# Optimization experiments

Hardware: AMD Instinct MI355X
Metric: run time of the kernel (lower is better)

The kernel has to match this reference:

```python
import jax, jax.numpy as jnp
import numpy as np

B, S = 4096, 256
D = 32  # output_size // 4


def setup_inputs() -> dict:
    key = jax.random.key(0)
    ks = jax.random.split(key, 32)
    # continuous features
    cont_p = jax.random.normal(ks[0], (B, S, 3), dtype=jnp.float32)
    cont_c = jax.random.normal(ks[1], (B, S, 2), dtype=jnp.float32)
    # categorical features, per-column vocab sizes from Embedding tables
    vocabs_p = [2, 2, 2, 11, 34]
    cat_p = jnp.stack([
        jax.random.randint(ks[2 + i], (B, S), 0, v, dtype=jnp.int32)
        for i, v in enumerate(vocabs_p)], axis=2)
    vocabs_c = [19, 31]
    cat_c = jnp.stack([
        jax.random.randint(ks[7 + i], (B, S), 0, v, dtype=jnp.int32)
        for i, v in enumerate(vocabs_c)], axis=2)
    lengths = jax.random.randint(ks[9], (B,), 1, S + 1, dtype=jnp.int32)

    def lin(k, fan_in, fan_out):
        bound = 1.0 / np.sqrt(fan_in)
        kw, kb = jax.random.split(k)
        w = jax.random.uniform(kw, (fan_in, fan_out), jnp.float32, -bound, bound)
        b = jax.random.uniform(kb, (fan_out,), jnp.float32, -bound, bound)
        return w, b

    w_p1, b_p1 = lin(ks[10], 3, D)
    w_p2, b_p2 = lin(ks[11], D, D)
    w_c1, b_c1 = lin(ks[12], 2, D)
    w_c2, b_c2 = lin(ks[13], D, D)
    emb_gender = jax.random.normal(ks[14], (2, D), dtype=jnp.float32)
    emb_korean = jax.random.normal(ks[15], (2, D), dtype=jnp.float32)
    emb_primary = jax.random.normal(ks[16], (2, D), dtype=jnp.float32)
    emb_job = jax.random.normal(ks[17], (11, D), dtype=jnp.float32)
    emb_rep = jax.random.normal(ks[18], (34, D), dtype=jnp.float32)
    emb_place = jax.random.normal(ks[19], (19, D), dtype=jnp.float32)
    emb_add = jax.random.normal(ks[20], (31, D), dtype=jnp.float32)
    w_fc1, b_fc1 = lin(ks[21], 128, 64)
    w_fc2, b_fc2 = lin(ks[22], 64, 2)

    return dict(cont_p=cont_p, cont_c=cont_c, cat_p=cat_p, cat_c=cat_c,
                lengths=lengths,
                w_p1=w_p1, b_p1=b_p1, w_p2=w_p2, b_p2=b_p2,
                w_c1=w_c1, b_c1=b_c1, w_c2=w_c2, b_c2=b_c2,
                emb_gender=emb_gender, emb_korean=emb_korean,
                emb_primary=emb_primary, emb_job=emb_job, emb_rep=emb_rep,
                emb_place=emb_place, emb_add=emb_add,
                w_fc1=w_fc1, b_fc1=b_fc1, w_fc2=w_fc2, b_fc2=b_fc2)


def reference(cont_p, cont_c, cat_p, cat_c, lengths,
              w_p1, b_p1, w_p2, b_p2, w_c1, b_c1, w_c2, b_c2,
              emb_gender, emb_korean, emb_primary, emb_job, emb_rep,
              emb_place, emb_add, w_fc1, b_fc1, w_fc2, b_fc2):
    # small per-token MLPs on continuous features -> [B,S,D]
    hp = jax.nn.relu(cont_p @ w_p1 + b_p1) @ w_p2 + b_p2
    hc = jax.nn.relu(cont_c @ w_c1 + b_c1) @ w_c2 + b_c2
    # multi-table embedding lookups, averaged per group -> [B,S,D]
    ep = (emb_gender[cat_p[:, :, 0]] + emb_korean[cat_p[:, :, 1]] +
          emb_primary[cat_p[:, :, 2]] + emb_job[cat_p[:, :, 3]] +
          emb_rep[cat_p[:, :, 4]]) / 5.0
    ec = (emb_place[cat_c[:, :, 0]] + emb_add[cat_c[:, :, 1]]) / 2.0
    # concat order matches torch: (cat_p, cat_c, cont_p, cont_c) -> [B,S,128]
    x = jnp.concatenate([ep, ec, hp, hc], axis=2)
    # ragged mean pool over first lengths[i] positions (masked segment mean)
    mask = (jnp.arange(x.shape[1])[None, :] < lengths[:, None])
    pooled = jnp.sum(x * mask[:, :, None], axis=1) / lengths[:, None].astype(x.dtype)
    # head: relu(fc1) -> relu(fc2); dropout p=0.0 is identity
    h = jax.nn.relu(pooled @ w_fc1 + b_fc1)
    return jax.nn.relu(h @ w_fc2 + b_fc2)
```

## Files before the change

### kernel.cpp

```cpp
#include <hip/hip_runtime.h>


#define BDIM 64

__global__ __launch_bounds__(BDIM, 4)
void mlpreg_kernel(const float* __restrict__ cont_p,
                   const float* __restrict__ cont_c,
                   const int* __restrict__ cat_p,
                   const int* __restrict__ cat_c,
                   const int* __restrict__ lengths,
                   const float* __restrict__ w_p1, const float* __restrict__ b_p1,
                   const float* __restrict__ w_p2, const float* __restrict__ b_p2,
                   const float* __restrict__ w_c1, const float* __restrict__ b_c1,
                   const float* __restrict__ w_c2, const float* __restrict__ b_c2,
                   const float* __restrict__ emb_g,  const float* __restrict__ emb_k,
                   const float* __restrict__ emb_pr, const float* __restrict__ emb_j,
                   const float* __restrict__ emb_r,  const float* __restrict__ emb_pl,
                   const float* __restrict__ emb_a,
                   const float* __restrict__ w_fc1, const float* __restrict__ b_fc1,
                   const float* __restrict__ w_fc2, const float* __restrict__ b_fc2,
                   float* __restrict__ out)
{
    constexpr int S = 256;
    __shared__ int   hist[96];
    __shared__ float sAcc[64];
    __shared__ float sPool[128];

    const int lane = threadIdx.x;
    const int b = blockIdx.x;
    const int ch = lane & 31, h = lane >> 5;

    int L = lengths[b]; L = (L < 1) ? 1 : (L > S ? S : L);
    const float Lf = (float)L, invL = 1.0f / Lf;

    hist[lane] = 0;
    if (lane < 32) hist[64 + lane] = 0;

    const float wp0 = w_p1[ch], wp1 = w_p1[32 + ch], wp2 = w_p1[64 + ch], bp = b_p1[ch];
    const float wc0 = w_c1[ch], wc1 = w_c1[32 + ch], bc = b_c1[ch];

    int sg = 0, sk = 0, sp = 0;
    {
        const int*  kp = cat_p + (size_t)b * (S * 5);
        const int2* kc = (const int2*)(cat_c + (size_t)b * (S * 2));
        #pragma unroll 2
        for (int t = lane; t < L; t += 64) {
            int v0 = kp[5 * t], v1 = kp[5 * t + 1], v2 = kp[5 * t + 2],
                v3 = kp[5 * t + 3], v4 = kp[5 * t + 4];
            int2 q = kc[t];
            sg += v0; sk += v1; sp += v2;
            atomicAdd(&hist[v3], 1);
            atomicAdd(&hist[11 + v4], 1);
            atomicAdd(&hist[45 + q.x], 1);
            atomicAdd(&hist[64 + q.y], 1);
        }
    }

    float aP = 0.f, aC = 0.f;
    {
        const float* tp = cont_p + (size_t)b * (S * 3);
        const float* tc = cont_c + (size_t)b * (S * 2);
        #pragma unroll 4
        for (int t = h; t < L; t += 2) {
            float c0 = tp[3 * t], c1 = tp[3 * t + 1], c2 = tp[3 * t + 2];
            float2 d2 = *(const float2*)&tc[2 * t];
            aP += fmaxf(fmaf(c0, wp0, fmaf(c1, wp1, fmaf(c2, wp2, bp))), 0.f);
            aC += fmaxf(fmaf(d2.x, wc0, fmaf(d2.y, wc1, bc)), 0.f);
        }
    }
    aP += __shfl_xor(aP, 32);
    aC += __shfl_xor(aC, 32);
    #pragma unroll
    for (int d = 32; d; d >>= 1) {
        sg += __shfl_xor(sg, d); sk += __shfl_xor(sk, d); sp += __shfl_xor(sp, d);
    }

    sAcc[lane] = (h ? aC : aP) * invL;
    __syncthreads();

    float A;
    {
        float fg = (float)sg, fk = (float)sk, fp = (float)sp;
        float g0 = emb_g[ch],  g1 = emb_g[32 + ch];
        float k0 = emb_k[ch],  k1 = emb_k[32 + ch];
        float p0 = emb_pr[ch], p1 = emb_pr[32 + ch];
        A = fmaf(Lf - fg, g0, fg * g1) + fmaf(Lf - fk, k0, fk * k1)
          + fmaf(Lf - fp, p0, fp * p1);
        A = h ? 0.f : A;
    }
    {
        const float* tA = h ? emb_pl : emb_j;
        const float* tB = h ? emb_a  : emb_r;
        const int nA = h ? 19 : 11;
        const int nT = h ? 50 : 45;
        const int hb = h ? 45 : 0;
        #pragma unroll 5
        for (int r = 0; r < nT; ++r) {
            const float* p = (r < nA) ? (tA + (r << 5)) : (tB + ((r - nA) << 5));
            A = fmaf((float)hist[hb + r], p[ch], A);
        }
        sPool[(h << 5) + ch] = A * (invL * (h ? 0.5f : 0.2f));
    }
    {
        const float* W2 = h ? w_c2 : w_p2;
        float v = (h ? b_c2 : b_p2)[ch];
        const float* acc = &sAcc[h << 5];
        #pragma unroll 8
        for (int k = 0; k < 32; ++k)
            v = fmaf(acc[k], W2[(k << 5) + ch], v);
        sPool[64 + (h << 5) + ch] = v;
    }
    __syncthreads();

    {
        float x = b_fc1[lane], y = 0.f;
        #pragma unroll 8
        for (int k = 0; k < 128; k += 4) {
            float4 u = *(const float4*)&sPool[k];
            float w0 = w_fc1[(size_t)(k    ) * 64 + lane];
            float w1 = w_fc1[(size_t)(k + 1) * 64 + lane];
            float w2 = w_fc1[(size_t)(k + 2) * 64 + lane];
            float w3 = w_fc1[(size_t)(k + 3) * 64 + lane];
            x = fmaf(u.x, w0, x); y = fmaf(u.y, w1, y);
            x = fmaf(u.z, w2, x); y = fmaf(u.w, w3, y);
        }
        float hv = fmaxf(x + y, 0.f);
        float q0 = hv * w_fc2[2 * lane], q1 = hv * w_fc2[2 * lane + 1];
        #pragma unroll
        for (int d = 32; d; d >>= 1) {
            q0 += __shfl_xor(q0, d); q1 += __shfl_xor(q1, d);
        }
        if (lane == 0) {
            float2 o2;
            o2.x = fmaxf(q0 + b_fc2[0], 0.f);
            o2.y = fmaxf(q1 + b_fc2[1], 0.f);
            *(float2*)&out[(size_t)b * 2] = o2;
        }
    }
}

extern "C" void kernel_launch(void* const* d_in, const int* in_sizes, int n_in,
                              void* d_out, int out_size, void* d_ws, size_t ws_size,
                              hipStream_t stream) {
    const float* cont_p = (const float*)d_in[0];
    const float* cont_c = (const float*)d_in[1];
    const int*   cat_p  = (const int*)d_in[2];
    const int*   cat_c  = (const int*)d_in[3];
    const int*   lens   = (const int*)d_in[4];
    const float* w_p1   = (const float*)d_in[5];
    const float* b_p1   = (const float*)d_in[6];
    const float* w_p2   = (const float*)d_in[7];
    const float* b_p2   = (const float*)d_in[8];
    const float* w_c1   = (const float*)d_in[9];
    const float* b_c1   = (const float*)d_in[10];
    const float* w_c2   = (const float*)d_in[11];
    const float* b_c2   = (const float*)d_in[12];
    const float* emb_g  = (const float*)d_in[13];
    const float* emb_k  = (const float*)d_in[14];
    const float* emb_pr = (const float*)d_in[15];
    const float* emb_j  = (const float*)d_in[16];
    const float* emb_r  = (const float*)d_in[17];
    const float* emb_pl = (const float*)d_in[18];
    const float* emb_a  = (const float*)d_in[19];
    const float* w_fc1  = (const float*)d_in[20];
    const float* b_fc1  = (const float*)d_in[21];
    const float* w_fc2  = (const float*)d_in[22];
    const float* b_fc2  = (const float*)d_in[23];
    float* out = (float*)d_out;

    hipLaunchKernelGGL(mlpreg_kernel, dim3(4096), dim3(BDIM), 0, stream,
                       cont_p, cont_c, cat_p, cat_c, lens,
                       w_p1, b_p1, w_p2, b_p2, w_c1, b_c1, w_c2, b_c2,
                       emb_g, emb_k, emb_pr, emb_j, emb_r, emb_pl, emb_a,
                       w_fc1, b_fc1, w_fc2, b_fc2, out);
}
```

Before: 155.2 us.

## Split sequence across four waves with direct global-to-LDS staging

Each batch row now uses 256 threads, with each wave taking a 64-token chunk. Its continuous and categorical inputs are copied straight into shared memory with global_load_lds 16-byte transfers and then read back as float4 vectors. The aim is more memory parallelism per row and coalesced wide loads in place of strided scalar loads. Partial sums are combined across waves through shared memory and the head runs on wave 0 only. This adds an extra barrier and idle waves for short sequences.

```diff
diff --git a/kernel.cpp b/kernel.cpp
--- a/kernel.cpp
+++ b/kernel.cpp
@@ -1,9 +1,15 @@
 #include <hip/hip_runtime.h>
 
 
-#define BDIM 64
-
-__global__ __launch_bounds__(BDIM, 4)
+#define BDIM 256
+
+__device__ __forceinline__ void gld16(const void* g, void* l) {
+    __builtin_amdgcn_global_load_lds((__attribute__((address_space(1))) void*)g,
+                                     (__attribute__((address_space(3))) void*)l,
+                                     16, 0, 0);
+}
+
+__global__ __launch_bounds__(BDIM)
 void mlpreg_kernel(const float* __restrict__ cont_p,
                    const float* __restrict__ cont_c,
                    const int* __restrict__ cat_p,
@@ -22,118 +28,171 @@
                    float* __restrict__ out)
 {
     constexpr int S = 256;
+    __shared__ __align__(16) float sPc[4][192];
+    __shared__ __align__(16) float sCc[4][128];
+    __shared__ __align__(16) int   sKp[4][320];
     __shared__ int   hist[96];
-    __shared__ float sAcc[64];
+    __shared__ float sAccW[4][64];
+    __shared__ int   sSums[4][3];
     __shared__ float sPool[128];
 
-    const int lane = threadIdx.x;
-    const int b = blockIdx.x;
-    const int ch = lane & 31, h = lane >> 5;
+    const int tid  = threadIdx.x;
+    const int wid  = tid >> 6;
+    const int lane = tid & 63;
+    const int ch   = lane & 31, h = lane >> 5;
+    const int b    = blockIdx.x;
 
     int L = lengths[b]; L = (L < 1) ? 1 : (L > S ? S : L);
     const float Lf = (float)L, invL = 1.0f / Lf;
 
-    hist[lane] = 0;
-    if (lane < 32) hist[64 + lane] = 0;
-
-    const float wp0 = w_p1[ch], wp1 = w_p1[32 + ch], wp2 = w_p1[64 + ch], bp = b_p1[ch];
-    const float wc0 = w_c1[ch], wc1 = w_c1[32 + ch], bc = b_c1[ch];
-
-    int sg = 0, sk = 0, sp = 0;
-    {
-        const int*  kp = cat_p + (size_t)b * (S * 5);
-        const int2* kc = (const int2*)(cat_c + (size_t)b * (S * 2));
-        #pragma unroll 2
-        for (int t = lane; t < L; t += 64) {
-            int v0 = kp[5 * t], v1 = kp[5 * t + 1], v2 = kp[5 * t + 2],
-                v3 = kp[5 * t + 3], v4 = kp[5 * t + 4];
-            int2 q = kc[t];
-            sg += v0; sk += v1; sp += v2;
-            atomicAdd(&hist[v3], 1);
-            atomicAdd(&hist[11 + v4], 1);
-            atomicAdd(&hist[45 + q.x], 1);
-            atomicAdd(&hist[64 + q.y], 1);
-        }
-    }
+    const int t0 = wid << 6;
+    const int nt = (L - t0 < 64) ? (L - t0) : 64;
+
+    if (tid < 96) hist[tid] = 0;
+
+    if (nt > 0) {
+        const char* gp = (const char*)(cont_p + (size_t)b * 768  + t0 * 3);
+        const char* gc = (const char*)(cont_c + (size_t)b * 512  + t0 * 2);
+        const char* gk = (const char*)(cat_p  + (size_t)b * 1280 + t0 * 5);
+        const int lo = 16 * lane;
+        const int bP = 12 * nt, bC = 8 * nt, bK = 20 * nt;
+        if (lo < bP)        gld16(gp + lo,        (char*)sPc[wid]);
+        if (lo < bC)        gld16(gc + lo,        (char*)sCc[wid]);
+        if (lo < bK)        gld16(gk + lo,        (char*)sKp[wid]);
+        if (1024 + lo < bK) gld16(gk + 1024 + lo, (char*)sKp[wid] + 1024);
+    }
+    int2 qc; qc.x = 0; qc.y = 0;
+    if (lane < nt) qc = ((const int2*)(cat_c + (size_t)b * 512))[t0 + lane];
+
+    const float wp0 = w_p1[ch], wp1v = w_p1[32 + ch], wp2v = w_p1[64 + ch], bp = b_p1[ch];
+    const float wc0 = w_c1[ch], wc1v = w_c1[32 + ch], bc = b_c1[ch];
+    float eg0 = 0, eg1 = 0, ek0 = 0, ek1 = 0, er0 = 0, er1 = 0;
+    float bias2 = 0, bf1 = 0, bq0 = 0, bq1 = 0;
+    float2 wf2; wf2.x = 0; wf2.y = 0;
+    if (wid == 0) {
+        eg0 = emb_g[ch];  eg1 = emb_g[32 + ch];
+        ek0 = emb_k[ch];  ek1 = emb_k[32 + ch];
+        er0 = emb_pr[ch]; er1 = emb_pr[32 + ch];
+        bias2 = h ? b_c2[ch] : b_p2[ch];
+        bf1 = b_fc1[lane];
+        wf2 = *(const float2*)&w_fc2[2 * lane];
+        bq0 = b_fc2[0]; bq1 = b_fc2[1];
+    }
+
+    __syncthreads();
 
     float aP = 0.f, aC = 0.f;
-    {
-        const float* tp = cont_p + (size_t)b * (S * 3);
-        const float* tc = cont_c + (size_t)b * (S * 2);
+    if (nt > 0) {
+        const int gf = nt >> 2;
+        const int gh = (gf + 1) >> 1;
+        const float4* tp4 = (const float4*)sPc[wid];
+        const float4* tc4 = (const float4*)sCc[wid];
         #pragma unroll 4
-        for (int t = h; t < L; t += 2) {
-            float c0 = tp[3 * t], c1 = tp[3 * t + 1], c2 = tp[3 * t + 2];
-            float2 d2 = *(const float2*)&tc[2 * t];
-            aP += fmaxf(fmaf(c0, wp0, fmaf(c1, wp1, fmaf(c2, wp2, bp))), 0.f);
-            aC += fmaxf(fmaf(d2.x, wc0, fmaf(d2.y, wc1, bc)), 0.f);
+        for (int i = 0; i < gh; ++i) {
+            const int g = h ? gh + i : i;
+            if (g < gf) {
+                float4 a  = tp4[3 * g], bb = tp4[3 * g + 1], cc = tp4[3 * g + 2];
+                float4 d  = tc4[2 * g], ee = tc4[2 * g + 1];
+                float p0 = fmaxf(fmaf(a.x,  wp0, fmaf(a.y,  wp1v, fmaf(a.z,  wp2v, bp))), 0.f);
+                float p1 = fmaxf(fmaf(a.w,  wp0, fmaf(bb.x, wp1v, fmaf(bb.y, wp2v, bp))), 0.f);
+                float p2 = fmaxf(fmaf(bb.z, wp0, fmaf(bb.w, wp1v, fmaf(cc.x, wp2v, bp))), 0.f);
+                float p3 = fmaxf(fmaf(cc.y, wp0, fmaf(cc.z, wp1v, fmaf(cc.w, wp2v, bp))), 0.f);
+                aP += (p0 + p1) + (p2 + p3);
+                float q0 = fmaxf(fmaf(d.x,  wc0, fmaf(d.y,  wc1v, bc)), 0.f);
+                float q1 = fmaxf(fmaf(d.z,  wc0, fmaf(d.w,  wc1v, bc)), 0.f);
+                float q2 = fmaxf(fmaf(ee.x, wc0, fmaf(ee.y, wc1v, bc)), 0.f);
+                float q3 = fmaxf(fmaf(ee.z, wc0, fmaf(ee.w, wc1v, bc)), 0.f);
+                aC += (q0 + q1) + (q2 + q3);
+            }
+        }
+        const int rem = nt & 3;
+        if (h == 0 && rem) {
+            const float* tp = sPc[wid] + 12 * gf;
+            const float* tc = sCc[wid] + 8 * gf;
+            for (int r = 0; r < rem; ++r) {
+                aP += fmaxf(fmaf(tp[3*r], wp0, fmaf(tp[3*r+1], wp1v, fmaf(tp[3*r+2], wp2v, bp))), 0.f);
+                aC += fmaxf(fmaf(tc[2*r], wc0, fmaf(tc[2*r+1], wc1v, bc)), 0.f);
+            }
         }
     }
     aP += __shfl_xor(aP, 32);
     aC += __shfl_xor(aC, 32);
+    sAccW[wid][lane] = h ? aC : aP;
+
+    int v0 = 0, v1 = 0, v2 = 0;
+    if (lane < nt) {
+        const int* kp = sKp[wid] + 5 * lane;
+        v0 = kp[0]; v1 = kp[1]; v2 = kp[2];
+        const int v3 = kp[3], v4 = kp[4];
+        atomicAdd(&hist[v3], 1);
+        atomicAdd(&hist[11 + v4], 1);
+        atomicAdd(&hist[45 + qc.x], 1);
+        atomicAdd(&hist[64 + qc.y], 1);
+    }
     #pragma unroll
     for (int d = 32; d; d >>= 1) {
-        sg += __shfl_xor(sg, d); sk += __shfl_xor(sk, d); sp += __shfl_xor(sp, d);
-    }
-
-    sAcc[lane] = (h ? aC : aP) * invL;
+        v0 += __shfl_xor(v0, d); v1 += __shfl_xor(v1, d); v2 += __shfl_xor(v2, d);
+    }
+    if (lane == 0) { sSums[wid][0] = v0; sSums[wid][1] = v1; sSums[wid][2] = v2; }
     __syncthreads();
 
-    float A;
-    {
-        float fg = (float)sg, fk = (float)sk, fp = (float)sp;
-        float g0 = emb_g[ch],  g1 = emb_g[32 + ch];
-        float k0 = emb_k[ch],  k1 = emb_k[32 + ch];
-        float p0 = emb_pr[ch], p1 = emb_pr[32 + ch];
-        A = fmaf(Lf - fg, g0, fg * g1) + fmaf(Lf - fk, k0, fk * k1)
-          + fmaf(Lf - fp, p0, fp * p1);
-        A = h ? 0.f : A;
-    }
-    {
-        const float* tA = h ? emb_pl : emb_j;
-        const float* tB = h ? emb_a  : emb_r;
-        const int nA = h ? 19 : 11;
-        const int nT = h ? 50 : 45;
-        const int hb = h ? 45 : 0;
-        #pragma unroll 5
-        for (int r = 0; r < nT; ++r) {
-            const float* p = (r < nA) ? (tA + (r << 5)) : (tB + ((r - nA) << 5));
-            A = fmaf((float)hist[hb + r], p[ch], A);
-        }
-        sPool[(h << 5) + ch] = A * (invL * (h ? 0.5f : 0.2f));
-    }
-    {
-        const float* W2 = h ? w_c2 : w_p2;
-        float v = (h ? b_c2 : b_p2)[ch];
-        const float* acc = &sAcc[h << 5];
+    if (wid == 0) {
+        const int sg = sSums[0][0] + sSums[1][0] + sSums[2][0] + sSums[3][0];
+        const int sk = sSums[0][1] + sSums[1][1] + sSums[2][1] + sSums[3][1];
+        const int sp = sSums[0][2] + sSums[1][2] + sSums[2][2] + sSums[3][2];
+        float A;
+        {
+            float fg = (float)sg, fk = (float)sk, fp = (float)sp;
+            A = fmaf(Lf - fg, eg0, fg * eg1) + fmaf(Lf - fk, ek0, fk * ek1)
+              + fmaf(Lf - fp, er0, fp * er1);
+            A = h ? 0.f : A;
+        }
+        {
+            const float* tA = h ? emb_pl : emb_j;
+            const float* tB = h ? emb_a  : emb_r;
+            const int nA = h ? 19 : 11;
+            const int nT = h ? 50 : 45;
+            const int hb = h ? 45 : 0;
+            #pragma unroll 5
+            for (int r = 0; r < nT; ++r) {
+                const float* p = (r < nA) ? (tA + (r << 5)) : (tB + ((r - nA) << 5));
+                A = fmaf((float)hist[hb + r], p[ch], A);
+            }
+            sPool[(h << 5) + ch] = A * (invL * (h ? 0.5f : 0.2f));
+        }
+        {
+            const float* W2 = h ? w_c2 : w_p2;
+            float vsum = 0.f;
+            #pragma unroll 8
+            for (int k = 0; k < 32; ++k) {
+                const int a = (h << 5) + k;
+                float ak = ((sAccW[0][a] + sAccW[1][a]) + (sAccW[2][a] + sAccW[3][a]));
+                vsum = fmaf(ak, W2[(k << 5) + ch], vsum);
+            }
+            sPool[64 + (h << 5) + ch] = fmaf(invL, vsum, bias2);
+        }
+    }
+    __syncthreads();
+
+    if (wid == 0) {
+        float x = bf1, y = 0.f;
         #pragma unroll 8
-        for (int k = 0; k < 32; ++k)
-            v = fmaf(acc[k], W2[(k << 5) + ch], v);
-        sPool[64 + (h << 5) + ch] = v;
-    }
-    __syncthreads();
-
-    {
-        float x = b_fc1[lane], y = 0.f;
-        #pragma unroll 8
-        for (int k = 0; k < 128; k += 4) {
-            float4 u = *(const float4*)&sPool[k];
-            float w0 = w_fc1[(size_t)(k    ) * 64 + lane];
+        for (int k = 0; k < 128; k += 2) {
+            float w0 = w_fc1[(size_t)k * 64 + lane];
             float w1 = w_fc1[(size_t)(k + 1) * 64 + lane];
-            float w2 = w_fc1[(size_t)(k + 2) * 64 + lane];
-            float w3 = w_fc1[(size_t)(k + 3) * 64 + lane];
+            float2 u = *(const float2*)&sPool[k];
             x = fmaf(u.x, w0, x); y = fmaf(u.y, w1, y);
-            x = fmaf(u.z, w2, x); y = fmaf(u.w, w3, y);
         }
         float hv = fmaxf(x + y, 0.f);
-        float q0 = hv * w_fc2[2 * lane], q1 = hv * w_fc2[2 * lane + 1];
+        float q0 = hv * wf2.x, q1 = hv * wf2.y;
         #pragma unroll
         for (int d = 32; d; d >>= 1) {
             q0 += __shfl_xor(q0, d); q1 += __shfl_xor(q1, d);
         }
         if (lane == 0) {
             float2 o2;
-            o2.x = fmaxf(q0 + b_fc2[0], 0.f);
-            o2.y = fmaxf(q1 + b_fc2[1], 0.f);
+            o2.x = fmaxf(q0 + bq0, 0.f);
+            o2.y = fmaxf(q1 + bq1, 0.f);
             *(float2*)&out[(size_t)b * 2] = o2;
         }
     }
```

Result: faster. 146.6 us (-5.6%).
